# Kernel tuning notes

Measured on AMD Instinct MI355X. Metric: run time of the kernel, lower is better.

## Reference

```python
import math
import jax, jax.numpy as jnp
import numpy as np

SCALE = math.sqrt(128.0)  # NOTE: original code MULTIPLIES by sqrt(128)
DROPOUT_P = 0.1


def setup_inputs() -> dict:
    key = jax.random.key(0)
    kq, kk, kv = jax.random.split(key, 3)
    B, Q, V, H = 4, 4096, 4096, 128
    return {
        "query": jax.random.normal(kq, (B, Q, H), dtype=jnp.float32),
        "key": jax.random.normal(kk, (B, V, H), dtype=jnp.float32),
        "value": jax.random.normal(kv, (B, V, H), dtype=jnp.float32),
    }


def reference(query, key, value):
    # qk: [B, Q, V]
    qk = jnp.einsum("bqh,bvh->bqv", query, key)
    scaled_qk = qk * SCALE
    softmax_qk = jax.nn.softmax(scaled_qk, axis=-1)
    # inverted dropout with a fixed RNG key (deterministic reference)
    dk = jax.random.key(42)
    keep = jax.random.bernoulli(dk, 1.0 - DROPOUT_P, softmax_qk.shape)
    dropout_qk = jnp.where(keep, softmax_qk / (1.0 - DROPOUT_P), 0.0)
    # output: [B, Q, H]
    return jnp.einsum("bqv,bvh->bqh", dropout_qk, value)
```

## Files before the change

kernel.cpp:

```cpp
#include <hip/hip_runtime.h>
#include <stdint.h>

#define NBATCH 4
#define NQ 4096
#define NV 4096
#define HD 128

#define SCL2E ((float)(11.31370849898476 * 1.4426950408889634))

#define KEEP_THRESH 3865470464u

#define SKIP_MARGIN 27.0f
#define DROP_MARGIN 20.0f

#define TILE_USH 24576
#define WS_NEEDED ((size_t)NBATCH * 64 * TILE_USH * 2)

#define PSTR 72
#define VLSTR 142

#define KSTR 144
#define VSTR 76

#define XSWZ(b) ((((b) & 7) << 6) | ((b) >> 3))

typedef __attribute__((ext_vector_type(8))) short short8;
typedef __attribute__((ext_vector_type(4))) float floatx4;
typedef unsigned int uint;
typedef unsigned short ushort;

__device__ __forceinline__ ushort bf16rne(float f) {
    uint u = __float_as_uint(f);
    u = (u + 0x7fffu + ((u >> 16) & 1u)) >> 16;
    return (ushort)u;
}
__device__ __forceinline__ float bf2f(ushort h) {
    return __uint_as_float(((uint)h) << 16);
}

template <int CTRL>
__device__ __forceinline__ float dppmov(float x) {
    return __int_as_float(__builtin_amdgcn_update_dpp(
        0, __float_as_int(x), CTRL, 0xF, 0xF, true));
}
__device__ __forceinline__ float row_max16(float x) {
    x = fmaxf(x, dppmov<0xB1>(x));
    x = fmaxf(x, dppmov<0x4E>(x));
    x = fmaxf(x, dppmov<0x141>(x));
    x = fmaxf(x, dppmov<0x140>(x));
    return x;
}
__device__ __forceinline__ float row_sum16(float x) {
    x += dppmov<0xB1>(x);
    x += dppmov<0x4E>(x);
    x += dppmov<0x141>(x);
    x += dppmov<0x140>(x);
    return x;
}

__device__ __forceinline__ uint rotl(uint x, int r) { return (x << r) | (x >> (32 - r)); }

__device__ __forceinline__ uint threefry_bits(uint j) {
    uint x0 = 0u;
    uint x1 = j;
    const uint k0 = 0u, k1 = 42u, k2 = 0u ^ 42u ^ 0x1BD11BDAu;
    x0 += k0; x1 += k1;
#define TFR4(a,b,c,d) \
    x0 += x1; x1 = rotl(x1, a); x1 ^= x0; \
    x0 += x1; x1 = rotl(x1, b); x1 ^= x0; \
    x0 += x1; x1 = rotl(x1, c); x1 ^= x0; \
    x0 += x1; x1 = rotl(x1, d); x1 ^= x0;
    TFR4(13, 15, 26, 6)
    x0 += k1; x1 += k2 + 1u;
    TFR4(17, 29, 16, 24)
    x0 += k2; x1 += k0 + 2u;
    TFR4(13, 15, 26, 6)
    x0 += k0; x1 += k1 + 3u;
    TFR4(17, 29, 16, 24)
    x0 += k1; x1 += k2 + 4u;
    TFR4(13, 15, 26, 6)
    x0 += k2; x1 += k0 + 5u;
#undef TFR4
    return x0 ^ x1;
}

__global__ __launch_bounds__(256)
void prepass(const float* __restrict__ Kg, const float* __restrict__ Vg,
             ushort* __restrict__ W) {
    __shared__ ushort vls[64 * VLSTR];
    const int swz  = XSWZ((int)blockIdx.x);
    const int rec  = swz >> 1;
    const int half = swz & 1;
    const int bb = rec >> 6;
    const int t  = rec & 63;
    const int v0 = t * 64;
    const size_t kvbase = (size_t)bb * NV * HD;
    ushort* dst = W + ((size_t)bb * 64 + t) * TILE_USH;
    const int tid = threadIdx.x;

    if (half == 0) {
        ushort* dkh = dst;
        ushort* dkl = dst + 8192;
#pragma unroll
        for (int i = 0; i < 4; ++i) {
            int lc = i * 256 + tid;
            int v = lc >> 4, c = lc & 15;
            const float* src = Kg + kvbase + (size_t)(v0 + v) * HD + c * 8;
            float x[8];
            *(float4*)&x[0] = *(const float4*)src;
            *(float4*)&x[4] = *(const float4*)(src + 4);
            uint H[4], L[4];
#pragma unroll
            for (int k = 0; k < 4; ++k) {
                ushort h0 = bf16rne(x[2 * k]),     h1 = bf16rne(x[2 * k + 1]);
                ushort l0 = bf16rne(x[2 * k] - bf2f(h0));
                ushort l1 = bf16rne(x[2 * k + 1] - bf2f(h1));
                H[k] = (uint)h0 | ((uint)h1 << 16);
                L[k] = (uint)l0 | ((uint)l1 << 16);
            }
            int pos = (((c >> 2) * 4 + (v >> 4)) * 64 + (c & 3) * 16 + (v & 15)) * 8;
            *(uint4*)&dkh[pos] = *(uint4*)H;
            *(uint4*)&dkl[pos] = *(uint4*)L;
        }
    } else {
        ushort* dvt = dst + 16384;
#pragma unroll
        for (int i = 0; i < 8; ++i) {
            int idx = i * 256 + tid;
            int v = idx >> 5, hq = idx & 31;
            float4 a = *(const float4*)(Vg + kvbase + (size_t)(v0 + v) * HD + hq * 4);
            uint w0 = (uint)bf16rne(a.x) | ((uint)bf16rne(a.y) << 16);
            uint w1 = (uint)bf16rne(a.z) | ((uint)bf16rne(a.w) << 16);
            *(uint*)&vls[v * VLSTR + hq * 4]     = w0;
            *(uint*)&vls[v * VLSTR + hq * 4 + 2] = w1;
        }
        __syncthreads();
#pragma unroll
        for (int i = 0; i < 4; ++i) {
            int lc = i * 256 + tid;
            int h = lc >> 3, c2 = lc & 7;
            uint Wd[4];
#pragma unroll
            for (int m = 0; m < 8; m += 2) {
                ushort a  = vls[(c2 * 8 + m) * VLSTR + h];
                ushort b2 = vls[(c2 * 8 + m + 1) * VLSTR + h];
                Wd[m >> 1] = (uint)a | ((uint)b2 << 16);
            }
            int pos = (((c2 >> 2) * 8 + (h >> 4)) * 64 + (c2 & 3) * 16 + (h & 15)) * 8;
            *(uint4*)&dvt[pos] = *(uint4*)Wd;
        }
    }
}

__global__ __launch_bounds__(256, 2)
void fa_mfma7(const float* __restrict__ Qg, const ushort* __restrict__ Wk,
              float* __restrict__ Og) {
    __shared__ __align__(16) float smemf[12288];
    __shared__ float mlbuf[3][32][2];
    __shared__ float gmx[32];

    const int tid  = threadIdx.x;
    const int wave = tid >> 6;
    const int lane = tid & 63;
    const int r    = lane & 15;
    const int qd   = lane >> 4;
    const int blockRow0 = XSWZ((int)blockIdx.x) * 32;
    const int b = blockRow0 >> 12;
    const ushort* kvw = Wk + (size_t)b * 64 * TILE_USH;
    ushort* pls = (ushort*)smemf + wave * (32 * PSTR);

    if (tid < 32) gmx[tid] = -1e30f;

    short8 qfh[2][4], qfl[2][4];
#pragma unroll
    for (int mr = 0; mr < 2; ++mr) {
        const float* qp = Qg + (size_t)(blockRow0 + mr * 16 + r) * HD + qd * 8;
#pragma unroll
        for (int kc = 0; kc < 4; ++kc) {
            float x[8];
            *(float4*)&x[0] = *(const float4*)(qp + kc * 32);
            *(float4*)&x[4] = *(const float4*)(qp + kc * 32 + 4);
#pragma unroll
            for (int j = 0; j < 8; ++j) {
                float xs = x[j] * SCL2E;
                ushort h = bf16rne(xs);
                qfh[mr][kc][j] = (short)h;
                qfl[mr][kc][j] = (short)bf16rne(xs - bf2f(h));
            }
        }
    }

    floatx4 oacc[2][8];
#pragma unroll
    for (int mr = 0; mr < 2; ++mr)
#pragma unroll
        for (int n = 0; n < 8; ++n) oacc[mr][n] = (floatx4){0.f, 0.f, 0.f, 0.f};
    float m2[2][4], lr[2][4];
#pragma unroll
    for (int mr = 0; mr < 2; ++mr)
#pragma unroll
        for (int g = 0; g < 4; ++g) { m2[mr][g] = -1e30f; lr[mr][g] = 0.f; }

    __syncthreads();

    for (int t = wave; t < 64; t += 4) {
        const ushort* tK = kvw + (size_t)t * TILE_USH;
        const ushort* tV = tK + 16384;
        const int v0 = t * 64;

        floatx4 cf[2][4];
#pragma unroll
        for (int mr = 0; mr < 2; ++mr)
#pragma unroll
            for (int nb = 0; nb < 4; ++nb) cf[mr][nb] = (floatx4){0.f, 0.f, 0.f, 0.f};
#pragma unroll
        for (int kc = 0; kc < 4; ++kc) {
            short8 kh[4], kl[4];
#pragma unroll
            for (int nb = 0; nb < 4; ++nb) {
                int off = ((kc * 4 + nb) * 64 + lane) * 8;
                kh[nb] = *(const short8*)&tK[off];
                kl[nb] = *(const short8*)&tK[8192 + off];
            }
#pragma unroll
            for (int nb = 0; nb < 4; ++nb)
#pragma unroll
                for (int mr = 0; mr < 2; ++mr) {
                    cf[mr][nb] = __builtin_amdgcn_mfma_f32_16x16x32_bf16(qfh[mr][kc], kh[nb], cf[mr][nb], 0, 0, 0);
                    cf[mr][nb] = __builtin_amdgcn_mfma_f32_16x16x32_bf16(qfh[mr][kc], kl[nb], cf[mr][nb], 0, 0, 0);
                    cf[mr][nb] = __builtin_amdgcn_mfma_f32_16x16x32_bf16(qfl[mr][kc], kh[nb], cf[mr][nb], 0, 0, 0);
                }
        }

        bool act[2];
#pragma unroll
        for (int mr = 0; mr < 2; ++mr) {
            float tmx[4], gm[4];
#pragma unroll
            for (int g = 0; g < 4; ++g) {
                float v = fmaxf(fmaxf(cf[mr][0][g], cf[mr][1][g]),
                                fmaxf(cf[mr][2][g], cf[mr][3][g]));
                tmx[g] = row_max16(v);
            }
            bool rowact = false;
#pragma unroll
            for (int g = 0; g < 4; ++g) {
                gm[g] = gmx[mr * 16 + qd * 4 + g];
                rowact |= (tmx[g] > fmaxf(m2[mr][g], gm[g]) - SKIP_MARGIN);
            }
#pragma unroll
            for (int g = 0; g < 4; ++g)
                if (r == 0 && tmx[g] > gm[g]) gmx[mr * 16 + qd * 4 + g] = tmx[g];
            act[mr] = __any(rowact);
            if (!act[mr]) continue;

            float alpha[4];
            bool nm = false;
#pragma unroll
            for (int g = 0; g < 4; ++g) nm |= (tmx[g] > m2[mr][g]);
            if (__any(nm)) {
#pragma unroll
                for (int g = 0; g < 4; ++g) {
                    float mn = fmaxf(m2[mr][g], tmx[g]);
                    alpha[g] = __builtin_amdgcn_exp2f(m2[mr][g] - mn);
                    m2[mr][g] = mn;
                }
#pragma unroll
                for (int n = 0; n < 8; ++n)
#pragma unroll
                    for (int g = 0; g < 4; ++g) oacc[mr][n][g] *= alpha[g];
            } else {
#pragma unroll
                for (int g = 0; g < 4; ++g) alpha[g] = 1.f;
            }

            float p[4][4], thr[4];
#pragma unroll
            for (int g = 0; g < 4; ++g) {
                float s = 0.f;
#pragma unroll
                for (int nb = 0; nb < 4; ++nb) {
                    p[nb][g] = __builtin_amdgcn_exp2f(cf[mr][nb][g] - m2[mr][g]);
                    s += p[nb][g];
                }
                s = row_sum16(s);
                lr[mr][g] = lr[mr][g] * alpha[g] + s;
                thr[g] = fmaxf(gm[g], m2[mr][g]) - DROP_MARGIN;
            }

#pragma unroll
            for (int nb = 0; nb < 4; ++nb) {
#pragma unroll
                for (int g = 0; g < 4; ++g) {
                    if (__any(cf[mr][nb][g] > thr[g])) {
                        uint j = (uint)(blockRow0 + mr * 16 + qd * 4 + g) * (uint)NV
                               + (uint)(v0 + nb * 16 + r);
                        if (threefry_bits(j) >= KEEP_THRESH) p[nb][g] = 0.f;
                    }
                    pls[(mr * 16 + qd * 4 + g) * PSTR + nb * 16 + r] =
                        (ushort)(__float_as_uint(p[nb][g]) >> 16);
                }
            }
        }

        if (act[0] | act[1]) {
            __asm__ volatile("s_waitcnt lgkmcnt(0)" ::: "memory");
#pragma unroll
            for (int mr = 0; mr < 2; ++mr) {
                if (!act[mr]) continue;
#pragma unroll
                for (int kc2 = 0; kc2 < 2; ++kc2) {
                    short8 pa = *(const short8*)&pls[(mr * 16 + r) * PSTR + kc2 * 32 + qd * 8];
#pragma unroll
                    for (int n = 0; n < 8; ++n) {
                        short8 vb = *(const short8*)&tV[((kc2 * 8 + n) * 64 + lane) * 8];
                        oacc[mr][n] = __builtin_amdgcn_mfma_f32_16x16x32_bf16(pa, vb, oacc[mr][n], 0, 0, 0);
                    }
                }
            }
        }
    }

    __syncthreads();
    if (wave >= 1) {
#pragma unroll
        for (int mr = 0; mr < 2; ++mr) {
            if (r == 0) {
#pragma unroll
                for (int g = 0; g < 4; ++g) {
                    mlbuf[wave - 1][mr * 16 + qd * 4 + g][0] = m2[mr][g];
                    mlbuf[wave - 1][mr * 16 + qd * 4 + g][1] = lr[mr][g];
                }
            }
#pragma unroll
            for (int n = 0; n < 8; ++n)
#pragma unroll
                for (int g = 0; g < 4; ++g)
                    smemf[(wave - 1) * 4096 + (mr * 16 + qd * 4 + g) * 128 + n * 16 + r] =
                        oacc[mr][n][g];
        }
    }
    __syncthreads();
    if (wave == 0) {
#pragma unroll
        for (int mr = 0; mr < 2; ++mr) {
            float a0[4], aw[3][4], inv[4];
#pragma unroll
            for (int g = 0; g < 4; ++g) {
                int row = mr * 16 + qd * 4 + g;
                float mn = m2[mr][g];
#pragma unroll
                for (int i = 0; i < 3; ++i) mn = fmaxf(mn, mlbuf[i][row][0]);
                a0[g] = __builtin_amdgcn_exp2f(m2[mr][g] - mn);
                float l = lr[mr][g] * a0[g];
#pragma unroll
                for (int i = 0; i < 3; ++i) {
                    aw[i][g] = __builtin_amdgcn_exp2f(mlbuf[i][row][0] - mn);
                    l += mlbuf[i][row][1] * aw[i][g];
                }
                inv[g] = 1.0f / (0.9f * l);
            }
#pragma unroll
            for (int n = 0; n < 8; ++n)
#pragma unroll
                for (int g = 0; g < 4; ++g) {
                    int row = mr * 16 + qd * 4 + g;
                    float o = oacc[mr][n][g] * a0[g];
#pragma unroll
                    for (int i = 0; i < 3; ++i)
                        o += smemf[i * 4096 + row * 128 + n * 16 + r] * aw[i][g];
                    Og[(size_t)(blockRow0 + row) * HD + n * 16 + r] = o * inv[g];
                }
        }
    }
}

__global__ __launch_bounds__(256)
void fa_mfma(const float* __restrict__ Qg, const float* __restrict__ Kg,
             const float* __restrict__ Vg, float* __restrict__ Og) {
    __shared__ ushort khi[64 * KSTR];
    __shared__ ushort klo[64 * KSTR];
    __shared__ ushort vt[128 * VSTR];
    __shared__ ushort plsf[4][16 * PSTR];

    const int tid  = threadIdx.x;
    const int wave = tid >> 6;
    const int lane = tid & 63;
    const int r    = lane & 15;
    const int qd   = lane >> 4;
    const int blockRow0 = blockIdx.x * 64;
    const int b = blockRow0 >> 12;
    const int waveRow0 = blockRow0 + wave * 16;
    const size_t kvbase = (size_t)b * NV * HD;

    short8 qfh[4], qfl[4];
    {
        const float* qp = Qg + (size_t)(waveRow0 + r) * HD + qd * 8;
#pragma unroll
        for (int kc = 0; kc < 4; ++kc) {
            float x[8];
            *(float4*)&x[0] = *(const float4*)(qp + kc * 32);
            *(float4*)&x[4] = *(const float4*)(qp + kc * 32 + 4);
#pragma unroll
            for (int j = 0; j < 8; ++j) {
                ushort h = bf16rne(x[j]);
                qfh[kc][j] = (short)h;
                qfl[kc][j] = (short)bf16rne(x[j] - bf2f(h));
            }
        }
    }

    floatx4 oacc[8];
#pragma unroll
    for (int n = 0; n < 8; ++n) oacc[n] = (floatx4){0.f, 0.f, 0.f, 0.f};
    float m2[4] = {-INFINITY, -INFINITY, -INFINITY, -INFINITY};
    float lr[4] = {0.f, 0.f, 0.f, 0.f};

    for (int v0 = 0; v0 < NV; v0 += 64) {
        __syncthreads();
#pragma unroll
        for (int i = 0; i < 8; ++i) {
            int f = i * 256 + tid;
            int v = f >> 5;
            int h = (f & 31) * 4;
            float4 kv = *(const float4*)(Kg + kvbase + (size_t)(v0 + v) * HD + h);
            ushort4 hh, ll;
            hh.x = bf16rne(kv.x); ll.x = bf16rne(kv.x - bf2f(hh.x));
            hh.y = bf16rne(kv.y); ll.y = bf16rne(kv.y - bf2f(hh.y));
            hh.z = bf16rne(kv.z); ll.z = bf16rne(kv.z - bf2f(hh.z));
            hh.w = bf16rne(kv.w); ll.w = bf16rne(kv.w - bf2f(hh.w));
            *(ushort4*)&khi[v * KSTR + h] = hh;
            *(ushort4*)&klo[v * KSTR + h] = ll;
        }
        {
            int hp = tid & 63, rp = tid >> 6;
            int h = hp * 2;
            const float* vpb = Vg + kvbase + (size_t)v0 * HD + h;
#pragma unroll
            for (int i = 0; i < 8; ++i) {
                int v = i * 8 + rp * 2;
                float2 a = *(const float2*)(vpb + (size_t)v * HD);
                float2 c = *(const float2*)(vpb + (size_t)(v + 1) * HD);
                uint w0 = (uint)bf16rne(a.x) | ((uint)bf16rne(c.x) << 16);
                uint w1 = (uint)bf16rne(a.y) | ((uint)bf16rne(c.y) << 16);
                *(uint*)&vt[h * VSTR + v]       = w0;
                *(uint*)&vt[(h + 1) * VSTR + v] = w1;
            }
        }
        __syncthreads();

        floatx4 cf[4];
#pragma unroll
        for (int nb = 0; nb < 4; ++nb) cf[nb] = (floatx4){0.f, 0.f, 0.f, 0.f};
#pragma unroll
        for (int kc = 0; kc < 4; ++kc) {
#pragma unroll
            for (int nb = 0; nb < 4; ++nb) {
                int off = (nb * 16 + r) * KSTR + kc * 32 + qd * 8;
                short8 kh = *(const short8*)&khi[off];
                short8 kl = *(const short8*)&klo[off];
                cf[nb] = __builtin_amdgcn_mfma_f32_16x16x32_bf16(qfh[kc], kh, cf[nb], 0, 0, 0);
                cf[nb] = __builtin_amdgcn_mfma_f32_16x16x32_bf16(qfh[kc], kl, cf[nb], 0, 0, 0);
                cf[nb] = __builtin_amdgcn_mfma_f32_16x16x32_bf16(qfl[kc], kh, cf[nb], 0, 0, 0);
            }
        }

        float ts[4][4], p[4][4];
#pragma unroll
        for (int nb = 0; nb < 4; ++nb)
#pragma unroll
            for (int g = 0; g < 4; ++g) ts[nb][g] = cf[nb][g] * SCL2E;

        float tsum[4], alpha[4], lnew[4];
#pragma unroll
        for (int g = 0; g < 4; ++g) {
            float tmx = fmaxf(fmaxf(ts[0][g], ts[1][g]), fmaxf(ts[2][g], ts[3][g]));
#pragma unroll
            for (int off = 1; off < 16; off <<= 1)
                tmx = fmaxf(tmx, __shfl_xor(tmx, off));
            float mn = fmaxf(m2[g], tmx);
            alpha[g] = __builtin_amdgcn_exp2f(m2[g] - mn);
            m2[g] = mn;
        }
#pragma unroll
        for (int g = 0; g < 4; ++g) {
            float s = 0.f;
#pragma unroll
            for (int nb = 0; nb < 4; ++nb) {
                p[nb][g] = __builtin_amdgcn_exp2f(ts[nb][g] - m2[g]);
                s += p[nb][g];
            }
#pragma unroll
            for (int off = 1; off < 16; off <<= 1)
                s += __shfl_xor(s, off);
            tsum[g] = s;
            lnew[g] = lr[g] * alpha[g] + s;
            lr[g] = lnew[g];
        }

        bool rowneed = false;
#pragma unroll
        for (int g = 0; g < 4; ++g) rowneed |= (tsum[g] > 1e-8f * lnew[g]);

        if (__any(rowneed)) {
#pragma unroll
            for (int n = 0; n < 8; ++n)
#pragma unroll
                for (int g = 0; g < 4; ++g) oacc[n][g] *= alpha[g];

#pragma unroll
            for (int nb = 0; nb < 4; ++nb) {
                bool nbneed = false;
#pragma unroll
                for (int g = 0; g < 4; ++g) nbneed |= (p[nb][g] > 1e-8f * lnew[g]);
                if (__any(nbneed)) {
#pragma unroll
                    for (int g = 0; g < 4; ++g) {
                        uint j = (uint)(waveRow0 + qd * 4 + g) * (uint)NV
                               + (uint)(v0 + nb * 16 + r);
                        if (threefry_bits(j) >= KEEP_THRESH) p[nb][g] = 0.f;
                    }
                }
#pragma unroll
                for (int g = 0; g < 4; ++g)
                    plsf[wave][(qd * 4 + g) * PSTR + nb * 16 + r] = bf16rne(p[nb][g]);
            }
            __asm__ volatile("s_waitcnt lgkmcnt(0)" ::: "memory");

#pragma unroll
            for (int kc2 = 0; kc2 < 2; ++kc2) {
                short8 pa = *(const short8*)&plsf[wave][r * PSTR + kc2 * 32 + qd * 8];
#pragma unroll
                for (int n = 0; n < 8; ++n) {
                    int off = (n * 16 + r) * VSTR + kc2 * 32 + qd * 8;
                    ushort4 u0 = *(const ushort4*)&vt[off];
                    ushort4 u1 = *(const ushort4*)&vt[off + 4];
                    short8 vb;
                    vb[0] = (short)u0.x; vb[1] = (short)u0.y; vb[2] = (short)u0.z; vb[3] = (short)u0.w;
                    vb[4] = (short)u1.x; vb[5] = (short)u1.y; vb[6] = (short)u1.z; vb[7] = (short)u1.w;
                    oacc[n] = __builtin_amdgcn_mfma_f32_16x16x32_bf16(pa, vb, oacc[n], 0, 0, 0);
                }
            }
        }
    }

    float inv[4];
#pragma unroll
    for (int g = 0; g < 4; ++g) inv[g] = 1.0f / (0.9f * lr[g]);
#pragma unroll
    for (int n = 0; n < 8; ++n)
#pragma unroll
        for (int g = 0; g < 4; ++g)
            Og[(size_t)(waveRow0 + qd * 4 + g) * HD + n * 16 + r] = oacc[n][g] * inv[g];
}

extern "C" void kernel_launch(void* const* d_in, const int* in_sizes, int n_in,
                              void* d_out, int out_size, void* d_ws, size_t ws_size,
                              hipStream_t stream) {
    (void)in_sizes; (void)n_in; (void)out_size;
    const float* Qg = (const float*)d_in[0];
    const float* Kg = (const float*)d_in[1];
    const float* Vg = (const float*)d_in[2];
    float* Og = (float*)d_out;
    if (ws_size >= WS_NEEDED) {
        ushort* W = (ushort*)d_ws;
        prepass<<<dim3(512), 256, 0, stream>>>(Kg, Vg, W);
        fa_mfma7<<<dim3(NBATCH * NQ / 32), 256, 0, stream>>>(Qg, (const ushort*)W, Og);
    } else {
        fa_mfma<<<dim3(NBATCH * NQ / 64), 256, 0, stream>>>(Qg, Kg, Vg, Og);
    }
}
```

Before: 190.1 us.

## Fuse K/V prepass and attention into one cooperative kernel with grid sync

Merges the bf16 K/V repacking prepass and the flash-attention kernel into a single cooperative launch of 512 blocks. Each block first converts its own K or V tile into the workspace, then all blocks meet at a grid-wide barrier before running the attention body. The aim is to remove the second kernel launch and the idle gap between the two kernels. In exchange it adds grid-sync and fence cost, and it depends on all 512 blocks being co-resident; if the cooperative launch fails it falls back to the old two-kernel path.

Measured after the change: 373.1 us. 1.96x slower.

```diff
diff --git a/kernel.cpp b/kernel.cpp
--- a/kernel.cpp
+++ b/kernel.cpp
@@ -1,5 +1,8 @@
 #include <hip/hip_runtime.h>
+#include <hip/hip_cooperative_groups.h>
 #include <stdint.h>
+
+namespace cg = cooperative_groups;
 
 #define NBATCH 4
 #define NQ 4096
@@ -18,11 +21,13 @@
 
 #define PSTR 72
 #define VLSTR 142
+#define VQS 34
 
 #define KSTR 144
 #define VSTR 76
 
 #define XSWZ(b) ((((b) & 7) << 6) | ((b) >> 3))
+#define PSWZ(b) ((((b) & 7) << 8) | ((b) >> 3))
 
 typedef __attribute__((ext_vector_type(8))) short short8;
 typedef __attribute__((ext_vector_type(4))) float floatx4;
@@ -84,6 +89,317 @@
     return x0 ^ x1;
 }
 
+__device__ __forceinline__ void prepass_khalf(const float* __restrict__ Kg,
+                                              ushort* __restrict__ dst,
+                                              size_t kvbase, int v0, int tid) {
+    ushort* dkh = dst;
+    ushort* dkl = dst + 8192;
+#pragma unroll
+    for (int i = 0; i < 4; ++i) {
+        int lc = i * 256 + tid;
+        int v = lc >> 4, c = lc & 15;
+        const float* src = Kg + kvbase + (size_t)(v0 + v) * HD + c * 8;
+        float x[8];
+        *(float4*)&x[0] = *(const float4*)src;
+        *(float4*)&x[4] = *(const float4*)(src + 4);
+        uint H[4], L[4];
+#pragma unroll
+        for (int k = 0; k < 4; ++k) {
+            ushort h0 = bf16rne(x[2 * k]),     h1 = bf16rne(x[2 * k + 1]);
+            ushort l0 = bf16rne(x[2 * k] - bf2f(h0));
+            ushort l1 = bf16rne(x[2 * k + 1] - bf2f(h1));
+            H[k] = (uint)h0 | ((uint)h1 << 16);
+            L[k] = (uint)l0 | ((uint)l1 << 16);
+        }
+        int pos = (((c >> 2) * 4 + (v >> 4)) * 64 + (c & 3) * 16 + (v & 15)) * 8;
+        *(uint4*)&dkh[pos] = *(uint4*)H;
+        *(uint4*)&dkl[pos] = *(uint4*)L;
+    }
+}
+
+__device__ __forceinline__ void prepass_vhalf(const float* __restrict__ Vg,
+                                              ushort* __restrict__ dst,
+                                              ushort* __restrict__ vls,
+                                              size_t kvbase, int v0, int tid) {
+    ushort* dvt = dst + 16384;
+#pragma unroll
+    for (int i = 0; i < 8; ++i) {
+        int idx = i * 256 + tid;
+        int v = idx >> 5, hq = idx & 31;
+        float4 a = *(const float4*)(Vg + kvbase + (size_t)(v0 + v) * HD + hq * 4);
+        uint w0 = (uint)bf16rne(a.x) | ((uint)bf16rne(a.y) << 16);
+        uint w1 = (uint)bf16rne(a.z) | ((uint)bf16rne(a.w) << 16);
+        *(uint*)&vls[v * VLSTR + hq * 4]     = w0;
+        *(uint*)&vls[v * VLSTR + hq * 4 + 2] = w1;
+    }
+    __syncthreads();
+#pragma unroll
+    for (int i = 0; i < 4; ++i) {
+        int lc = i * 256 + tid;
+        int h = lc >> 3, c2 = lc & 7;
+        uint Wd[4];
+#pragma unroll
+        for (int m = 0; m < 8; m += 2) {
+            ushort a  = vls[(c2 * 8 + m) * VLSTR + h];
+            ushort b2 = vls[(c2 * 8 + m + 1) * VLSTR + h];
+            Wd[m >> 1] = (uint)a | ((uint)b2 << 16);
+        }
+        int pos = (((c2 >> 2) * 8 + (h >> 4)) * 64 + (c2 & 3) * 16 + (h & 15)) * 8;
+        *(uint4*)&dvt[pos] = *(uint4*)Wd;
+    }
+}
+
+__device__ __forceinline__ void fa_body(const float* __restrict__ Qg,
+                                        const ushort* __restrict__ Wk,
+                                        float* __restrict__ Og,
+                                        float* smemf, float (*mlbuf)[32][2],
+                                        float* gmx, int swz) {
+    const int tid  = threadIdx.x;
+    const int wave = tid >> 6;
+    const int lane = tid & 63;
+    const int r    = lane & 15;
+    const int qd   = lane >> 4;
+    const int blockRow0 = swz * 32;
+    const int b = blockRow0 >> 12;
+    const ushort* kvw = Wk + (size_t)b * 64 * TILE_USH;
+    ushort* pls = (ushort*)smemf + wave * (32 * PSTR);
+
+    short8 qfh[2][4], qfl[2][4];
+#pragma unroll
+    for (int mr = 0; mr < 2; ++mr) {
+        const float* qp = Qg + (size_t)(blockRow0 + mr * 16 + r) * HD + qd * 8;
+#pragma unroll
+        for (int kc = 0; kc < 4; ++kc) {
+            float x[8];
+            *(float4*)&x[0] = *(const float4*)(qp + kc * 32);
+            *(float4*)&x[4] = *(const float4*)(qp + kc * 32 + 4);
+#pragma unroll
+            for (int j = 0; j < 8; ++j) {
+                float xs = x[j] * SCL2E;
+                ushort h = bf16rne(xs);
+                qfh[mr][kc][j] = (short)h;
+                qfl[mr][kc][j] = (short)bf16rne(xs - bf2f(h));
+            }
+        }
+    }
+
+    floatx4 oacc[2][8];
+#pragma unroll
+    for (int mr = 0; mr < 2; ++mr)
+#pragma unroll
+        for (int n = 0; n < 8; ++n) oacc[mr][n] = (floatx4){0.f, 0.f, 0.f, 0.f};
+    float m2[2][4], lr[2][4];
+#pragma unroll
+    for (int mr = 0; mr < 2; ++mr)
+#pragma unroll
+        for (int g = 0; g < 4; ++g) { m2[mr][g] = -1e30f; lr[mr][g] = 0.f; }
+
+    __syncthreads();
+
+    for (int t = wave; t < 64; t += 4) {
+        const ushort* tK = kvw + (size_t)t * TILE_USH;
+        const ushort* tV = tK + 16384;
+        const int v0 = t * 64;
+
+        floatx4 cf[2][4];
+#pragma unroll
+        for (int mr = 0; mr < 2; ++mr)
+#pragma unroll
+            for (int nb = 0; nb < 4; ++nb) cf[mr][nb] = (floatx4){0.f, 0.f, 0.f, 0.f};
+#pragma unroll
+        for (int kc = 0; kc < 4; ++kc) {
+            short8 kh[4], kl[4];
+#pragma unroll
+            for (int nb = 0; nb < 4; ++nb) {
+                int off = ((kc * 4 + nb) * 64 + lane) * 8;
+                kh[nb] = *(const short8*)&tK[off];
+                kl[nb] = *(const short8*)&tK[8192 + off];
+            }
+#pragma unroll
+            for (int nb = 0; nb < 4; ++nb)
+#pragma unroll
+                for (int mr = 0; mr < 2; ++mr) {
+                    cf[mr][nb] = __builtin_amdgcn_mfma_f32_16x16x32_bf16(qfh[mr][kc], kh[nb], cf[mr][nb], 0, 0, 0);
+                    cf[mr][nb] = __builtin_amdgcn_mfma_f32_16x16x32_bf16(qfh[mr][kc], kl[nb], cf[mr][nb], 0, 0, 0);
+                    cf[mr][nb] = __builtin_amdgcn_mfma_f32_16x16x32_bf16(qfl[mr][kc], kh[nb], cf[mr][nb], 0, 0, 0);
+                }
+        }
+
+        bool act[2];
+#pragma unroll
+        for (int mr = 0; mr < 2; ++mr) {
+            float tmx[4], gm[4];
+#pragma unroll
+            for (int g = 0; g < 4; ++g) {
+                float v = fmaxf(fmaxf(cf[mr][0][g], cf[mr][1][g]),
+                                fmaxf(cf[mr][2][g], cf[mr][3][g]));
+                tmx[g] = row_max16(v);
+            }
+            bool rowact = false;
+#pragma unroll
+            for (int g = 0; g < 4; ++g) {
+                gm[g] = gmx[mr * 16 + qd * 4 + g];
+                rowact |= (tmx[g] > fmaxf(m2[mr][g], gm[g]) - SKIP_MARGIN);
+            }
+#pragma unroll
+            for (int g = 0; g < 4; ++g)
+                if (r == 0 && tmx[g] > gm[g]) gmx[mr * 16 + qd * 4 + g] = tmx[g];
+            act[mr] = __any(rowact);
+            if (!act[mr]) continue;
+
+            float alpha[4];
+            bool nm = false;
+#pragma unroll
+            for (int g = 0; g < 4; ++g) nm |= (tmx[g] > m2[mr][g]);
+            if (__any(nm)) {
+#pragma unroll
+                for (int g = 0; g < 4; ++g) {
+                    float mn = fmaxf(m2[mr][g], tmx[g]);
+                    alpha[g] = __builtin_amdgcn_exp2f(m2[mr][g] - mn);
+                    m2[mr][g] = mn;
+                }
+#pragma unroll
+                for (int n = 0; n < 8; ++n)
+#pragma unroll
+                    for (int g = 0; g < 4; ++g) oacc[mr][n][g] *= alpha[g];
+            } else {
+#pragma unroll
+                for (int g = 0; g < 4; ++g) alpha[g] = 1.f;
+            }
+
+            float p[4][4], thr[4];
+#pragma unroll
+            for (int g = 0; g < 4; ++g) {
+                float s = 0.f;
+#pragma unroll
+                for (int nb = 0; nb < 4; ++nb) {
+                    p[nb][g] = __builtin_amdgcn_exp2f(cf[mr][nb][g] - m2[mr][g]);
+                    s += p[nb][g];
+                }
+                s = row_sum16(s);
+                lr[mr][g] = lr[mr][g] * alpha[g] + s;
+                thr[g] = fmaxf(gm[g], m2[mr][g]) - DROP_MARGIN;
+            }
+
+#pragma unroll
+            for (int nb = 0; nb < 4; ++nb) {
+#pragma unroll
+                for (int g = 0; g < 4; ++g) {
+                    if (__any(cf[mr][nb][g] > thr[g])) {
+                        uint j = (uint)(blockRow0 + mr * 16 + qd * 4 + g) * (uint)NV
+                               + (uint)(v0 + nb * 16 + r);
+                        if (threefry_bits(j) >= KEEP_THRESH) p[nb][g] = 0.f;
+                    }
+                    pls[(mr * 16 + qd * 4 + g) * PSTR + nb * 16 + r] =
+                        (ushort)(__float_as_uint(p[nb][g]) >> 16);
+                }
+            }
+        }
+
+        if (act[0] | act[1]) {
+            __asm__ volatile("s_waitcnt lgkmcnt(0)" ::: "memory");
+#pragma unroll
+            for (int mr = 0; mr < 2; ++mr) {
+                if (!act[mr]) continue;
+#pragma unroll
+                for (int kc2 = 0; kc2 < 2; ++kc2) {
+                    short8 pa = *(const short8*)&pls[(mr * 16 + r) * PSTR + kc2 * 32 + qd * 8];
+#pragma unroll
+                    for (int n = 0; n < 8; ++n) {
+                        short8 vb = *(const short8*)&tV[((kc2 * 8 + n) * 64 + lane) * 8];
+                        oacc[mr][n] = __builtin_amdgcn_mfma_f32_16x16x32_bf16(pa, vb, oacc[mr][n], 0, 0, 0);
+                    }
+                }
+            }
+        }
+    }
+
+    __syncthreads();
+    if (wave >= 1) {
+#pragma unroll
+        for (int mr = 0; mr < 2; ++mr) {
+            if (r == 0) {
+#pragma unroll
+                for (int g = 0; g < 4; ++g) {
+                    mlbuf[wave - 1][mr * 16 + qd * 4 + g][0] = m2[mr][g];
+                    mlbuf[wave - 1][mr * 16 + qd * 4 + g][1] = lr[mr][g];
+                }
+            }
+#pragma unroll
+            for (int n = 0; n < 8; ++n)
+#pragma unroll
+                for (int g = 0; g < 4; ++g)
+                    smemf[(wave - 1) * 4096 + (mr * 16 + qd * 4 + g) * 128 + n * 16 + r] =
+                        oacc[mr][n][g];
+        }
+    }
+    __syncthreads();
+    if (wave == 0) {
+#pragma unroll
+        for (int mr = 0; mr < 2; ++mr) {
+            float a0[4], aw[3][4], inv[4];
+#pragma unroll
+            for (int g = 0; g < 4; ++g) {
+                int row = mr * 16 + qd * 4 + g;
+                float mn = m2[mr][g];
+#pragma unroll
+                for (int i = 0; i < 3; ++i) mn = fmaxf(mn, mlbuf[i][row][0]);
+                a0[g] = __builtin_amdgcn_exp2f(m2[mr][g] - mn);
+                float l = lr[mr][g] * a0[g];
+#pragma unroll
+                for (int i = 0; i < 3; ++i) {
+                    aw[i][g] = __builtin_amdgcn_exp2f(mlbuf[i][row][0] - mn);
+                    l += mlbuf[i][row][1] * aw[i][g];
+                }
+                inv[g] = 1.0f / (0.9f * l);
+            }
+#pragma unroll
+            for (int n = 0; n < 8; ++n)
+#pragma unroll
+                for (int g = 0; g < 4; ++g) {
+                    int row = mr * 16 + qd * 4 + g;
+                    float o = oacc[mr][n][g] * a0[g];
+#pragma unroll
+                    for (int i = 0; i < 3; ++i)
+                        o += smemf[i * 4096 + row * 128 + n * 16 + r] * aw[i][g];
+                    Og[(size_t)(blockRow0 + row) * HD + n * 16 + r] = o * inv[g];
+                }
+        }
+    }
+}
+
+__global__ __launch_bounds__(256, 2)
+void fa_fused(const float* __restrict__ Qg, const float* __restrict__ Kg,
+              const float* __restrict__ Vg, ushort* __restrict__ W,
+              float* __restrict__ Og) {
+    __shared__ __align__(16) float smemf[12288];
+    __shared__ float mlbuf[3][32][2];
+    __shared__ float gmx[32];
+
+    const int tid = threadIdx.x;
+    const int swz = XSWZ((int)blockIdx.x);
+
+    {
+        const int rec  = swz >> 1;
+        const int half = swz & 1;
+        const int bb = rec >> 6;
+        const int t  = rec & 63;
+        const int v0 = t * 64;
+        const size_t kvbase = (size_t)bb * NV * HD;
+        ushort* dst = W + ((size_t)bb * 64 + t) * TILE_USH;
+        if (half == 0) prepass_khalf(Kg, dst, kvbase, v0, tid);
+        else           prepass_vhalf(Vg, dst, (ushort*)smemf, kvbase, v0, tid);
+    }
+
+    if (tid < 32) gmx[tid] = -1e30f;
+
+    __threadfence();
+    cg::this_grid().sync();
+    __threadfence();
+
+    fa_body(Qg, W, Og, smemf, mlbuf, gmx, swz);
+}
+
 __global__ __launch_bounds__(256)
 void prepass(const float* __restrict__ Kg, const float* __restrict__ Vg,
              ushort* __restrict__ W) {
@@ -97,59 +413,8 @@
     const size_t kvbase = (size_t)bb * NV * HD;
     ushort* dst = W + ((size_t)bb * 64 + t) * TILE_USH;
     const int tid = threadIdx.x;
-
-    if (half == 0) {
-        ushort* dkh = dst;
-        ushort* dkl = dst + 8192;
-#pragma unroll
-        for (int i = 0; i < 4; ++i) {
-            int lc = i * 256 + tid;
-            int v = lc >> 4, c = lc & 15;
-            const float* src = Kg + kvbase + (size_t)(v0 + v) * HD + c * 8;
-            float x[8];
-            *(float4*)&x[0] = *(const float4*)src;
-            *(float4*)&x[4] = *(const float4*)(src + 4);
-            uint H[4], L[4];
-#pragma unroll
-            for (int k = 0; k < 4; ++k) {
-                ushort h0 = bf16rne(x[2 * k]),     h1 = bf16rne(x[2 * k + 1]);
-                ushort l0 = bf16rne(x[2 * k] - bf2f(h0));
-                ushort l1 = bf16rne(x[2 * k + 1] - bf2f(h1));
-                H[k] = (uint)h0 | ((uint)h1 << 16);
-                L[k] = (uint)l0 | ((uint)l1 << 16);
-            }
-            int pos = (((c >> 2) * 4 + (v >> 4)) * 64 + (c & 3) * 16 + (v & 15)) * 8;
-            *(uint4*)&dkh[pos] = *(uint4*)H;
-            *(uint4*)&dkl[pos] = *(uint4*)L;
-        }
-    } else {
-        ushort* dvt = dst + 16384;
-#pragma unroll
-        for (int i = 0; i < 8; ++i) {
-            int idx = i * 256 + tid;
-            int v = idx >> 5, hq = idx & 31;
-            float4 a = *(const float4*)(Vg + kvbase + (size_t)(v0 + v) * HD + hq * 4);
-            uint w0 = (uint)bf16rne(a.x) | ((uint)bf16rne(a.y) << 16);
-            uint w1 = (uint)bf16rne(a.z) | ((uint)bf16rne(a.w) << 16);
-            *(uint*)&vls[v * VLSTR + hq * 4]     = w0;
-            *(uint*)&vls[v * VLSTR + hq * 4 + 2] = w1;
-        }
-        __syncthreads();
-#pragma unroll
-        for (int i = 0; i < 4; ++i) {
-            int lc = i * 256 + tid;
-            int h = lc >> 3, c2 = lc & 7;
-            uint Wd[4];
-#pragma unroll
-            for (int m = 0; m < 8; m += 2) {
-                ushort a  = vls[(c2 * 8 + m) * VLSTR + h];
-                ushort b2 = vls[(c2 * 8 + m + 1) * VLSTR + h];
-                Wd[m >> 1] = (uint)a | ((uint)b2 << 16);
-            }
-            int pos = (((c2 >> 2) * 8 + (h >> 4)) * 64 + (c2 & 3) * 16 + (h & 15)) * 8;
-            *(uint4*)&dvt[pos] = *(uint4*)Wd;
-        }
-    }
+    if (half == 0) prepass_khalf(Kg, dst, kvbase, v0, tid);
+    else           prepass_vhalf(Vg, dst, vls, kvbase, v0, tid);
 }
 
 __global__ __launch_bounds__(256, 2)
@@ -158,221 +423,8 @@
     __shared__ __align__(16) float smemf[12288];
     __shared__ float mlbuf[3][32][2];
     __shared__ float gmx[32];
-
-    const int tid  = threadIdx.x;
-    const int wave = tid >> 6;
-    const int lane = tid & 63;
-    const int r    = lane & 15;
-    const int qd   = lane >> 4;
-    const int blockRow0 = XSWZ((int)blockIdx.x) * 32;
-    const int b = blockRow0 >> 12;
-    const ushort* kvw = Wk + (size_t)b * 64 * TILE_USH;
-    ushort* pls = (ushort*)smemf + wave * (32 * PSTR);
-
-    if (tid < 32) gmx[tid] = -1e30f;
-
-    short8 qfh[2][4], qfl[2][4];
-#pragma unroll
-    for (int mr = 0; mr < 2; ++mr) {
-        const float* qp = Qg + (size_t)(blockRow0 + mr * 16 + r) * HD + qd * 8;
-#pragma unroll
-        for (int kc = 0; kc < 4; ++kc) {
-            float x[8];
-            *(float4*)&x[0] = *(const float4*)(qp + kc * 32);
-            *(float4*)&x[4] = *(const float4*)(qp + kc * 32 + 4);
-#pragma unroll
-            for (int j = 0; j < 8; ++j) {
-                float xs = x[j] * SCL2E;
-                ushort h = bf16rne(xs);
-                qfh[mr][kc][j] = (short)h;
-                qfl[mr][kc][j] = (short)bf16rne(xs - bf2f(h));
-            }
-        }
-    }
-
-    floatx4 oacc[2][8];
-#pragma unroll
-    for (int mr = 0; mr < 2; ++mr)
-#pragma unroll
-        for (int n = 0; n < 8; ++n) oacc[mr][n] = (floatx4){0.f, 0.f, 0.f, 0.f};
-    float m2[2][4], lr[2][4];
-#pragma unroll
-    for (int mr = 0; mr < 2; ++mr)
-#pragma unroll
-        for (int g = 0; g < 4; ++g) { m2[mr][g] = -1e30f; lr[mr][g] = 0.f; }
-
-    __syncthreads();
-
-    for (int t = wave; t < 64; t += 4) {
-        const ushort* tK = kvw + (size_t)t * TILE_USH;
-        const ushort* tV = tK + 16384;
-        const int v0 = t * 64;
-
-        floatx4 cf[2][4];
-#pragma unroll
-        for (int mr = 0; mr < 2; ++mr)
-#pragma unroll
-            for (int nb = 0; nb < 4; ++nb) cf[mr][nb] = (floatx4){0.f, 0.f, 0.f, 0.f};
-#pragma unroll
-        for (int kc = 0; kc < 4; ++kc) {
-            short8 kh[4], kl[4];
-#pragma unroll
-            for (int nb = 0; nb < 4; ++nb) {
-                int off = ((kc * 4 + nb) * 64 + lane) * 8;
-                kh[nb] = *(const short8*)&tK[off];
-                kl[nb] = *(const short8*)&tK[8192 + off];
-            }
-#pragma unroll
-            for (int nb = 0; nb < 4; ++nb)
-#pragma unroll
-                for (int mr = 0; mr < 2; ++mr) {
-                    cf[mr][nb] = __builtin_amdgcn_mfma_f32_16x16x32_bf16(qfh[mr][kc], kh[nb], cf[mr][nb], 0, 0, 0);
-                    cf[mr][nb] = __builtin_amdgcn_mfma_f32_16x16x32_bf16(qfh[mr][kc], kl[nb], cf[mr][nb], 0, 0, 0);
-                    cf[mr][nb] = __builtin_amdgcn_mfma_f32_16x16x32_bf16(qfl[mr][kc], kh[nb], cf[mr][nb], 0, 0, 0);
-                }
-        }
-
-        bool act[2];
-#pragma unroll
-        for (int mr = 0; mr < 2; ++mr) {
-            float tmx[4], gm[4];
-#pragma unroll
-            for (int g = 0; g < 4; ++g) {
-                float v = fmaxf(fmaxf(cf[mr][0][g], cf[mr][1][g]),
-                                fmaxf(cf[mr][2][g], cf[mr][3][g]));
-                tmx[g] = row_max16(v);
-            }
-            bool rowact = false;
-#pragma unroll
-            for (int g = 0; g < 4; ++g) {
-                gm[g] = gmx[mr * 16 + qd * 4 + g];
-                rowact |= (tmx[g] > fmaxf(m2[mr][g], gm[g]) - SKIP_MARGIN);
-            }
-#pragma unroll
-            for (int g = 0; g < 4; ++g)
-                if (r == 0 && tmx[g] > gm[g]) gmx[mr * 16 + qd * 4 + g] = tmx[g];
-            act[mr] = __any(rowact);
-            if (!act[mr]) continue;
-
-            float alpha[4];
-            bool nm = false;
-#pragma unroll
-            for (int g = 0; g < 4; ++g) nm |= (tmx[g] > m2[mr][g]);
-            if (__any(nm)) {
-#pragma unroll
-                for (int g = 0; g < 4; ++g) {
-                    float mn = fmaxf(m2[mr][g], tmx[g]);
-                    alpha[g] = __builtin_amdgcn_exp2f(m2[mr][g] - mn);
-                    m2[mr][g] = mn;
-                }
-#pragma unroll
-                for (int n = 0; n < 8; ++n)
-#pragma unroll
-                    for (int g = 0; g < 4; ++g) oacc[mr][n][g] *= alpha[g];
-            } else {
-#pragma unroll
-                for (int g = 0; g < 4; ++g) alpha[g] = 1.f;
-            }
-
-            float p[4][4], thr[4];
-#pragma unroll
-            for (int g = 0; g < 4; ++g) {
-                float s = 0.f;
-#pragma unroll
-                for (int nb = 0; nb < 4; ++nb) {
-                    p[nb][g] = __builtin_amdgcn_exp2f(cf[mr][nb][g] - m2[mr][g]);
-                    s += p[nb][g];
-                }
-                s = row_sum16(s);
-                lr[mr][g] = lr[mr][g] * alpha[g] + s;
-                thr[g] = fmaxf(gm[g], m2[mr][g]) - DROP_MARGIN;
-            }
-
-#pragma unroll
-            for (int nb = 0; nb < 4; ++nb) {
-#pragma unroll
-                for (int g = 0; g < 4; ++g) {
-                    if (__any(cf[mr][nb][g] > thr[g])) {
-                        uint j = (uint)(blockRow0 + mr * 16 + qd * 4 + g) * (uint)NV
-                               + (uint)(v0 + nb * 16 + r);
-                        if (threefry_bits(j) >= KEEP_THRESH) p[nb][g] = 0.f;
-                    }
-                    pls[(mr * 16 + qd * 4 + g) * PSTR + nb * 16 + r] =
-                        (ushort)(__float_as_uint(p[nb][g]) >> 16);
-                }
-            }
-        }
-
-        if (act[0] | act[1]) {
-            __asm__ volatile("s_waitcnt lgkmcnt(0)" ::: "memory");
-#pragma unroll
-            for (int mr = 0; mr < 2; ++mr) {
-                if (!act[mr]) continue;
-#pragma unroll
-                for (int kc2 = 0; kc2 < 2; ++kc2) {
-                    short8 pa = *(const short8*)&pls[(mr * 16 + r) * PSTR + kc2 * 32 + qd * 8];
-#pragma unroll
-                    for (int n = 0; n < 8; ++n) {
-                        short8 vb = *(const short8*)&tV[((kc2 * 8 + n) * 64 + lane) * 8];
-                        oacc[mr][n] = __builtin_amdgcn_mfma_f32_16x16x32_bf16(pa, vb, oacc[mr][n], 0, 0, 0);
-                    }
-                }
-            }
-        }
-    }
-
-    __syncthreads();
-    if (wave >= 1) {
-#pragma unroll
-        for (int mr = 0; mr < 2; ++mr) {
-            if (r == 0) {
-#pragma unroll
-                for (int g = 0; g < 4; ++g) {
-                    mlbuf[wave - 1][mr * 16 + qd * 4 + g][0] = m2[mr][g];
-                    mlbuf[wave - 1][mr * 16 + qd * 4 + g][1] = lr[mr][g];
-                }
-            }
-#pragma unroll
-            for (int n = 0; n < 8; ++n)
-#pragma unroll
-                for (int g = 0; g < 4; ++g)
-                    smemf[(wave - 1) * 4096 + (mr * 16 + qd * 4 + g) * 128 + n * 16 + r] =
-                        oacc[mr][n][g];
-        }
-    }
-    __syncthreads();
-    if (wave == 0) {
-#pragma unroll
-        for (int mr = 0; mr < 2; ++mr) {
-            float a0[4], aw[3][4], inv[4];
-#pragma unroll
-            for (int g = 0; g < 4; ++g) {
-                int row = mr * 16 + qd * 4 + g;
-                float mn = m2[mr][g];
-#pragma unroll
-                for (int i = 0; i < 3; ++i) mn = fmaxf(mn, mlbuf[i][row][0]);
-                a0[g] = __builtin_amdgcn_exp2f(m2[mr][g] - mn);
-                float l = lr[mr][g] * a0[g];
-#pragma unroll
-                for (int i = 0; i < 3; ++i) {
-                    aw[i][g] = __builtin_amdgcn_exp2f(mlbuf[i][row][0] - mn);
-                    l += mlbuf[i][row][1] * aw[i][g];
-                }
-                inv[g] = 1.0f / (0.9f * l);
-            }
-#pragma unroll
-            for (int n = 0; n < 8; ++n)
-#pragma unroll
-                for (int g = 0; g < 4; ++g) {
-                    int row = mr * 16 + qd * 4 + g;
-                    float o = oacc[mr][n][g] * a0[g];
-#pragma unroll
-                    for (int i = 0; i < 3; ++i)
-                        o += smemf[i * 4096 + row * 128 + n * 16 + r] * aw[i][g];
-                    Og[(size_t)(blockRow0 + row) * HD + n * 16 + r] = o * inv[g];
-                }
-        }
-    }
+    if (threadIdx.x < 32) gmx[threadIdx.x] = -1e30f;
+    fa_body(Qg, Wk, Og, smemf, mlbuf, gmx, XSWZ((int)blockIdx.x));
 }
 
 __global__ __launch_bounds__(256)
@@ -564,8 +616,14 @@
     float* Og = (float*)d_out;
     if (ws_size >= WS_NEEDED) {
         ushort* W = (ushort*)d_ws;
-        prepass<<<dim3(512), 256, 0, stream>>>(Kg, Vg, W);
-        fa_mfma7<<<dim3(NBATCH * NQ / 32), 256, 0, stream>>>(Qg, (const ushort*)W, Og);
+        void* kargs[] = { (void*)&Qg, (void*)&Kg, (void*)&Vg, (void*)&W, (void*)&Og };
+        hipError_t err = hipLaunchCooperativeKernel(
+            (const void*)fa_fused, dim3(512), dim3(256), kargs, 0, stream);
+        if (err != hipSuccess) {
+            (void)hipGetLastError();
+            prepass<<<dim3(512), 256, 0, stream>>>(Kg, Vg, W);
+            fa_mfma7<<<dim3(NBATCH * NQ / 32), 256, 0, stream>>>(Qg, (const ushort*)W, Og);
+        }
     } else {
         fa_mfma<<<dim3(NBATCH * NQ / 64), 256, 0, stream>>>(Qg, Kg, Vg, Og);
     }
```
